# Optimization experiments

Hardware: AMD Instinct MI355X
Metric: run time of the kernel (lower is better)

## Reference

```python
import jax, jax.numpy as jnp
import numpy as np

B, C, L, M, EMB, HID = 32, 64, 8192, 32, 256, 64

def setup_inputs() -> dict:
    key = jax.random.key(0)
    ks = jax.random.split(key, 14)
    s_w = 1.0 / (C * C)
    s_a = 1.0 / EMB
    return {
        "x": jax.random.normal(ks[0], (B, C, L), jnp.float32),
        "emb": jax.random.normal(ks[1], (B, EMB), jnp.float32),
        "weights_pos": s_w * jax.random.normal(ks[2], (C, C, M, 2), jnp.float32),
        "weights_neg": s_w * jax.random.normal(ks[3], (C, C, M, 2), jnp.float32),
        "A_real_pos": s_a * jax.random.normal(ks[4], (M, EMB), jnp.float32),
        "A_imag_pos": s_a * jax.random.normal(ks[5], (M, EMB), jnp.float32),
        "A_real_neg": s_a * jax.random.normal(ks[6], (M, EMB), jnp.float32),
        "A_imag_neg": s_a * jax.random.normal(ks[7], (M, EMB), jnp.float32),
        "tm_w1": 0.05 * jax.random.normal(ks[8], (HID, EMB), jnp.float32),
        "tm_b1": jnp.zeros((HID,), jnp.float32),
        "tm_w2": 0.05 * jax.random.normal(ks[9], (2 * C, HID), jnp.float32),
        "tm_b2": jnp.zeros((2 * C,), jnp.float32),
        "lin_w": 0.05 * jax.random.normal(ks[10], (C, C), jnp.float32),
        "lin_b": jnp.zeros((C,), jnp.float32),
    }

def reference(x, emb, weights_pos, weights_neg, A_real_pos, A_imag_pos,
              A_real_neg, A_imag_neg, tm_w1, tm_b1, tm_w2, tm_b2, lin_w, lin_b):
    b, c, l = x.shape
    m = weights_pos.shape[2]
    k = l // 2 + 1
    # ---- SpectralConv1d branch ----
    x_ft = jnp.fft.rfft(x, norm="ortho")  # [B,C,K] complex
    wp = weights_pos[..., 0] + 1j * weights_pos[..., 1]  # [Ci,Co,M]
    wn = weights_neg[..., 0] + 1j * weights_neg[..., 1]
    phi_p = (emb @ A_real_pos.T) + 1j * (emb @ A_imag_pos.T)  # [B,M]
    phi_n = (emb @ A_real_neg.T) + 1j * (emb @ A_imag_neg.T)
    out_pos = jnp.einsum("bim,iom->bom", x_ft[:, :, :m], wp) * phi_p[:, None, :]
    out_neg = jnp.einsum("bim,iom->bom", x_ft[:, :, k - m:], wn) * phi_n[:, None, :]
    out_ft = jnp.zeros((b, c, k), dtype=x_ft.dtype)
    out_ft = out_ft.at[:, :, :m].set(out_pos).at[:, :, k - m:].set(out_neg)
    x1 = jnp.fft.irfft(out_ft, n=l, norm="ortho")  # [B,C,L]
    # ---- Conv1DTime branch (FiLM-style) ----
    h = jax.nn.silu(emb @ tm_w1.T + tm_b1)          # [B,HID]
    gb = h @ tm_w2.T + tm_b2                         # [B,2C]
    gamma, beta = gb[:, :c], gb[:, c:]
    xl = jnp.einsum("bcl,oc->bol", x, lin_w) + lin_b[None, :, None]
    x2 = xl * (1.0 + gamma[:, :, None]) + beta[:, :, None]
    return jax.nn.silu(x1 + x2)
```

## Files before the change

### kernel.cpp

```cpp
#include <hip/hip_runtime.h>
#include <math.h>

#define L_ 8192
#define EMB_ 256
#define HID_ 64

typedef __attribute__((ext_vector_type(8))) short bf16x8;
typedef __attribute__((ext_vector_type(4))) float f32x4;
typedef __attribute__((ext_vector_type(4))) int i32x4;

#define OFF_TFB  0
#define OFF_TLB  262144
#define OFF_AFB  524288
#define OFF_XFRP 917504
#define OFF_B2   3014656
#define OFF_PHI  3016704
#define OFF_GB   3020800
#define OFF_WT   3024896
#define OFF_XT   3549184

__device__ inline int pkbf(float a, float b) {
    int r;
    asm volatile("v_cvt_pk_bf16_f32 %0, %1, %2" : "=v"(r) : "v"(a), "v"(b));
    return r;
}
__device__ inline bf16x8 asbf(i32x4 v) { union { i32x4 i; bf16x8 h; } u; u.i = v; return u.h; }
#define MFMA(A,B,C) __builtin_amdgcn_mfma_f32_16x16x32_bf16((A),(B),(C),0,0,0)

__device__ inline ushort f2bf(float v) {
    unsigned b = __float_as_uint(v);
    return (ushort)((b + 0x7FFFu + ((b >> 16) & 1u)) >> 16);
}
__device__ inline float bf2f(ushort h) { return __uint_as_float(((unsigned)h) << 16); }
__device__ inline float hwsin(float rev) { float r; asm("v_sin_f32 %0, %1" : "=v"(r) : "v"(rev)); return r; }
__device__ inline float hwcos(float rev) { float r; asm("v_cos_f32 %0, %1" : "=v"(r) : "v"(rev)); return r; }
__device__ inline unsigned permb(unsigned hi, unsigned lo, unsigned sel) {
    unsigned r;
    asm("v_perm_b32 %0, %1, %2, %3" : "=v"(r) : "v"(hi), "v"(lo), "v"(sel));
    return r;
}

__global__ __launch_bounds__(256) void k_init(ushort* __restrict__ TLB, ushort* __restrict__ TFB,
        const float* __restrict__ emb,
        const float* __restrict__ Arp, const float* __restrict__ Aip,
        const float* __restrict__ Arn, const float* __restrict__ Ain, float* __restrict__ phi,
        const float* __restrict__ w1, const float* __restrict__ b1,
        const float* __restrict__ w2, const float* __restrict__ b2, float* __restrict__ gb,
        const float* __restrict__ wpos, const float* __restrict__ wneg, float* __restrict__ WT) {
    int bid = blockIdx.x;
    if (bid < 4096) {
        int idx = bid * 256 + threadIdx.x;
        int f, l; ushort* dst;
        if (idx < 524288) {
            int u = idx;
            int e = u & 7, lane = (u >> 3) & 63, ct = (u >> 9) & 3, kstep = u >> 11;
            l = kstep * 32 + ((lane >> 4) << 3) + e;
            f = ct * 16 + (lane & 15);
            dst = TLB + u;
        } else {
            int u = idx - 524288;
            int e = u & 7, lane = (u >> 3) & 63, ts = (u >> 9) & 1, lt = u >> 10;
            l = lt * 16 + (lane & 15);
            f = ts * 32 + ((lane >> 4) << 3) + e;
            dst = TFB + u;
        }
        int fr = f & 31; bool sinp = (f & 32) != 0;
        int r = (fr * l) & (L_ - 1);
        float rev = (float)r * (1.0f / (float)L_);
        float v = sinp ? hwsin(rev) : hwcos(rev);
        *dst = f2bf(v);
    } else if (bid < 4112) {
        int tid = (bid - 4096) * 256 + threadIdx.x;
        int b = tid >> 7;
        int mm = (tid >> 2) & 31;
        int cmp = tid & 3;
        const float* A = (cmp == 0) ? Arp : (cmp == 1) ? Aip : (cmp == 2) ? Arn : Ain;
        const float4* e4 = (const float4*)(emb + b * EMB_);
        const float4* a4 = (const float4*)(A + mm * EMB_);
        float acc = 0.f;
        for (int q = 0; q < EMB_ / 4; ++q) {
            float4 ev = e4[q], av = a4[q];
            acc += ev.x * av.x + ev.y * av.y + ev.z * av.z + ev.w * av.w;
        }
        phi[tid] = acc;
    } else if (bid < 4144) {
        __shared__ float h[HID_];
        int b = bid - 4112, t = threadIdx.x;
        if (t < HID_) {
            const float4* e4 = (const float4*)(emb + b * EMB_);
            const float4* w4 = (const float4*)(w1 + t * EMB_);
            float acc = b1[t];
            for (int q = 0; q < EMB_ / 4; ++q) {
                float4 ev = e4[q], wv = w4[q];
                acc += ev.x * wv.x + ev.y * wv.y + ev.z * wv.z + ev.w * wv.w;
            }
            h[t] = acc / (1.f + expf(-acc));
        }
        __syncthreads();
        if (t < 128) {
            float g = b2[t];
            const float4* h4 = (const float4*)h;
            const float4* w4 = (const float4*)(w2 + t * HID_);
            for (int q = 0; q < HID_ / 4; ++q) {
                float4 hv = h4[q], wv = w4[q];
                g += hv.x * wv.x + hv.y * wv.y + hv.z * wv.z + hv.w * wv.w;
            }
            if (t < 64) gb[(b * 64 + t) * 2 + 0] = 1.f + g;
            else        gb[(b * 64 + (t - 64)) * 2 + 1] = g;
        }
    } else {
        int t = bid - 4144;
        int side = t >> 6, i = t & 63;
        const float* W = side ? wneg : wpos;
        const float* src = W + (size_t)i * 4096;
        int tid = threadIdx.x;
        #pragma unroll
        for (int j = 0; j < 8; ++j) {
            int u = tid + 256 * j;
            int mm = u >> 6, o = u & 63;
            float2 v = *(const float2*)(src + o * 64 + mm * 2);
            *(float2*)(WT + ((size_t)(side * 32 + mm)) * 8192 + i * 128 + o * 2) = v;
        }
    }
}

__global__ __launch_bounds__(256, 4) void k_dft(const float* __restrict__ x,
        const ushort* __restrict__ TLB, float* __restrict__ xfrp, unsigned* __restrict__ XT2) {
    __shared__ float sP[4][16][132];
    int stripe = blockIdx.x >> 3;
    int lseg = blockIdx.x & 7;
    int w = threadIdx.x >> 6;
    int lane = threadIdx.x & 63;
    int row = lane & 15, koff = (lane >> 4) << 3;
    int r0 = stripe * 16;
    int kb0 = lseg * 1024 + w * 256;

    f32x4 acc[8];
    #pragma unroll
    for (int i = 0; i < 8; ++i) acc[i] = (f32x4){0.f, 0.f, 0.f, 0.f};

    const float* ap = x + (size_t)(r0 + row) * L_ + kb0 + koff;
    const i32x4* tb = (const i32x4*)TLB;
    int tbase = (kb0 >> 5) * 256 + lane;
    const i32x4 SM = {(int)0x80000000, (int)0x80000000, (int)0x80000000, (int)0x80000000};
    unsigned* xtb = XT2 + ((size_t)stripe * 4096 + ((kb0 + koff) >> 1)) * 16 + row;

    float4 xa0 = *(const float4*)(ap);
    float4 xc0 = *(const float4*)(ap + 4);
    float4 xa1 = *(const float4*)(ap + 32);
    float4 xc1 = *(const float4*)(ap + 36);
    float4 xa2 = *(const float4*)(ap + 64);
    float4 xc2 = *(const float4*)(ap + 68);
    i32x4 t0 = tb[tbase], t1 = tb[tbase + 64], t2 = tb[tbase + 128], t3 = tb[tbase + 192];
    i32x4 u0 = tb[tbase + 256], u1 = tb[tbase + 320], u2 = tb[tbase + 384], u3 = tb[tbase + 448];
    #pragma unroll
    for (int ks = 0; ks < 8; ++ks) {
        float4 nxa = {0,0,0,0}, nxc = {0,0,0,0};
        i32x4 v0 = u0, v1 = u1, v2 = u2, v3 = u3;
        if (ks < 5) {
            nxa = *(const float4*)(ap + (ks + 3) * 32);
            nxc = *(const float4*)(ap + (ks + 3) * 32 + 4);
        }
        if (ks < 6) {
            int ti = tbase + (ks + 2) * 256;
            v0 = tb[ti]; v1 = tb[ti + 64]; v2 = tb[ti + 128]; v3 = tb[ti + 192];
        }
        int h0 = pkbf(xa0.x, xa0.y), h1 = pkbf(xa0.z, xa0.w);
        int h2 = pkbf(xc0.x, xc0.y), h3 = pkbf(xc0.z, xc0.w);
        bf16x8 AH = asbf((i32x4){h0, h1, h2, h3});
        acc[0] = MFMA(AH, asbf(t0), acc[0]); acc[4] = MFMA(AH, asbf(t0 ^ SM), acc[4]);
        acc[1] = MFMA(AH, asbf(t1), acc[1]); acc[5] = MFMA(AH, asbf(t1 ^ SM), acc[5]);
        acc[2] = MFMA(AH, asbf(t2), acc[2]); acc[6] = MFMA(AH, asbf(t2 ^ SM), acc[6]);
        acc[3] = MFMA(AH, asbf(t3), acc[3]); acc[7] = MFMA(AH, asbf(t3 ^ SM), acc[7]);
        {
            unsigned* xtp = xtb + (size_t)(ks * 16) * 16;
            xtp[0]  = (unsigned)h0;
            xtp[16] = (unsigned)h1;
            xtp[32] = (unsigned)h2;
            xtp[48] = (unsigned)h3;
        }
        xa0 = xa1; xc0 = xc1; xa1 = xa2; xc1 = xc2; xa2 = nxa; xc2 = nxc;
        t0 = u0; t1 = u1; t2 = u2; t3 = u3;
        u0 = v0; u1 = v1; u2 = v2; u3 = v3;
    }
    int crow = (lane >> 4) << 2;
    int ccol = lane & 15;
    #pragma unroll
    for (int ct = 0; ct < 8; ++ct)
        #pragma unroll
        for (int r = 0; r < 4; ++r)
            sP[w][crow + r][ct * 16 + ccol] = acc[ct][r];
    __syncthreads();
    #pragma unroll
    for (int i = 0; i < 8; ++i) {
        int e = threadIdx.x + 256 * i;
        int rr = e & 15, cc = e >> 4;
        float s = sP[0][rr][cc] + sP[1][rr][cc] + sP[2][rr][cc] + sP[3][rr][cc];
        xfrp[((size_t)(lseg * 128 + cc)) * 2048 + r0 + rr] = s;
    }
}

__global__ __launch_bounds__(256) void k_mix(const float* __restrict__ xfrt,
        const float* __restrict__ WT,
        const float* __restrict__ phi, const float* __restrict__ lw,
        const float* __restrict__ lb, const float* __restrict__ gb,
        ushort* __restrict__ afb, float* __restrict__ bias2) {
    int bi = blockIdx.x;
    int tid = threadIdx.x;
    if (bi >= 256) {
        int b = bi - 256;
        ushort* dst = afb + (size_t)b * 24576;
        #pragma unroll
        for (int j = 0; j < 16; ++j) {
            int u = tid + 256 * j;
            int e = u & 7, lane = (u >> 3) & 63, mt = (u >> 9) & 3, ks2 = u >> 11;
            int c = mt * 16 + (lane & 15);
            int kk = ((lane >> 4) << 3) + e;
            float v = lw[c * 64 + ks2 * 32 + kk] * gb[(b * 64 + c) * 2];
            ushort hi = f2bf(v);
            int base = (((4 + ks2) * 4 + mt) * 64 + lane) * 16;
            dst[base + e] = hi;
            dst[base + 8 + e] = f2bf(v - bf2f(hi));
        }
        if (tid < 64) {
            float g1 = gb[(b * 64 + tid) * 2], be = gb[(b * 64 + tid) * 2 + 1];
            bias2[b * 64 + tid] = lb[tid] * g1 + be;
        }
        return;
    }
    __shared__ float sW[64][64][2];
    __shared__ float sXr[8][64], sXi[8][64];
    int bh = bi & 3, side = (bi >> 2) & 1, mm = bi >> 3;
    int slot = side ? (31 - mm) : mm;
    int colR = side ? (64 + slot) : mm;
    int colI = side ? (96 + slot) : (32 + mm);

    {
        const float4* wt = (const float4*)(WT + ((size_t)(side * 32 + mm)) * 8192);
        float* sWlin = &sW[0][0][0];
        #pragma unroll
        for (int j = 0; j < 8; ++j) {
            int u = tid + 256 * j;
            *(float4*)&sWlin[u * 4] = wt[u];
        }
    }
    {
        const float2* pR = (const float2*)(xfrt + (size_t)colR * 2048 + bh * 512);
        const float2* pI = (const float2*)(xfrt + (size_t)colI * 2048 + bh * 512);
        float2 aR = {0, 0}, aI = {0, 0};
        #pragma unroll
        for (int s = 0; s < 8; ++s) {
            float2 vR = pR[(size_t)s * 131072 + tid];
            float2 vI = pI[(size_t)s * 131072 + tid];
            aR.x += vR.x; aR.y += vR.y;
            aI.x += vI.x; aI.y += vI.y;
        }
        if (!side) { aI.x = -aI.x; aI.y = -aI.y; }
        *(float2*)&sXr[tid >> 5][(tid & 31) * 2] = aR;
        *(float2*)&sXi[tid >> 5][(tid & 31) * 2] = aI;
    }
    __syncthreads();

    int o = tid & 63, bg = tid >> 6;
    const float invL = 1.f / (float)L_;
    float fac = (slot == 0) ? invL : 2.f * invL;
    int comp = side ? 2 : 0;
    int e = slot & 7, kgrp = slot >> 3;
    int mt = o >> 4, lane = kgrp * 16 + (o & 15);
    #pragma unroll
    for (int bl = 0; bl < 2; ++bl) {
        int b_local = bg * 2 + bl;
        int b = bh * 8 + b_local;
        float sre = 0.f, sim = 0.f;
        #pragma unroll 16
        for (int i = 0; i < 64; ++i) {
            float wr = sW[i][o][0], wi = sW[i][o][1];
            float xr = sXr[b_local][i], xi = sXi[b_local][i];
            sre += xr * wr - xi * wi;
            sim += xr * wi + xi * wr;
        }
        const float* ph = &phi[(b * 32 + mm) * 4 + (side ? 2 : 0)];
        float phr = ph[0], phim = ph[1];
        float Pre = sre * phr - sim * phim;
        float Pim = sre * phim + sim * phr;
        float a = fac * Pre;
        float bcoef = (slot == 0) ? 0.f : (side ? 2.f * invL * Pim : -2.f * invL * Pim);
        ushort* dst = afb + (size_t)b * 24576;
        ushort hiA = f2bf(a);
        int baseA = ((comp * 4 + mt) * 64 + lane) * 16;
        dst[baseA + e] = hiA;
        dst[baseA + 8 + e] = f2bf(a - bf2f(hiA));
        ushort hiB = f2bf(bcoef);
        int baseB = (((comp + 1) * 4 + mt) * 64 + lane) * 16;
        dst[baseB + e] = hiB;
        dst[baseB + 8 + e] = f2bf(bcoef - bf2f(hiB));
    }
}

#define TPART(ts)                                                                        \
    {                                                                                    \
        i32x4 bh_[2];                                                                    \
        _Pragma("unroll")                                                                \
        for (int nj = 0; nj < 2; ++nj)                                                   \
            bh_[nj] = tb[((lt0 + nj) * 2 + (ts)) * 64 + lane];                           \
        _Pragma("unroll")                                                                \
        for (int mt = 0; mt < 4; ++mt) {                                                 \
            i32x4 ah0 = ab[(((ts) * 4 + mt) * 64 + lane) * 2];                           \
            i32x4 ah1 = ab[(((2 + (ts)) * 4 + mt) * 64 + lane) * 2];                     \
            bf16x8 AH0 = asbf(ah0), AH1 = asbf(ah1);                                     \
            _Pragma("unroll")                                                            \
            for (int nj = 0; nj < 2; ++nj) {                                             \
                acc[mt][nj] = MFMA(AH0, asbf(bh_[nj]), acc[mt][nj]);                     \
                acc[mt][nj] = MFMA(AH1, asbf(bh_[nj] ^ SM), acc[mt][nj]);                \
            }                                                                            \
        }                                                                                \
    }

#define XPART(ts, xv0, xv1)                                                              \
    {                                                                                    \
        bf16x8 XH0 = asbf(xv0), XH1 = asbf(xv1);                                         \
        _Pragma("unroll")                                                                \
        for (int mt = 0; mt < 4; ++mt) {                                                 \
            i32x4 ah = ab[(((4 + (ts)) * 4 + mt) * 64 + lane) * 2];                      \
            bf16x8 AH = asbf(ah);                                                        \
            acc[mt][0] = MFMA(AH, XH0, acc[mt][0]);                                      \
            acc[mt][1] = MFMA(AH, XH1, acc[mt][1]);                                      \
        }                                                                                \
    }

#define XEXTRACT(q0, q1, dstvar)                                                         \
    dstvar = (i32x4){                                                                    \
        (int)permb((unsigned)q0[1], (unsigned)q0[0], sel),                               \
        (int)permb((unsigned)q0[3], (unsigned)q0[2], sel),                               \
        (int)permb((unsigned)q1[1], (unsigned)q1[0], sel),                               \
        (int)permb((unsigned)q1[3], (unsigned)q1[2], sel)};

__global__ __launch_bounds__(256, 3) void k_fuse(const unsigned* __restrict__ XT2,
        const ushort* __restrict__ TFB, const ushort* __restrict__ AFB,
        const float* __restrict__ bias2, float* __restrict__ out) {
    int b = blockIdx.x >> 6, lt = blockIdx.x & 63;
    int w = threadIdx.x >> 6, lane = threadIdx.x & 63;
    int col = lane & 15, kgrp = lane >> 4;
    int lbase = lt * 128 + w * 32;
    int lt0 = lbase >> 4;
    const i32x4* tb = (const i32x4*)TFB;
    const i32x4* ab = (const i32x4*)AFB + (size_t)b * 3072;
    const i32x4* xt4 = (const i32x4*)XT2;

    f32x4 acc[4][2];
    #pragma unroll
    for (int i = 0; i < 4; ++i)
        #pragma unroll
        for (int j = 0; j < 2; ++j) acc[i][j] = (f32x4){0.f, 0.f, 0.f, 0.f};

    int sm = (col & 1) ? (int)0x80008000 : 0;
    i32x4 SM = {sm, sm, sm, sm};
    unsigned sel = (col & 1) ? 0x07060302u : 0x05040100u;

    size_t i00 = ((size_t)(b * 4 + (kgrp >> 1)) * 4096 + ((lbase + col) >> 1)) * 4 + (kgrp & 1) * 2;
    size_t i01 = i00 + 8 * 4;
    size_t i10 = i00 + (size_t)2 * 4096 * 4;
    size_t i11 = i10 + 8 * 4;
    i32x4 q000 = xt4[i00], q001 = xt4[i00 + 1];
    i32x4 q010 = xt4[i01], q011 = xt4[i01 + 1];
    i32x4 q100 = xt4[i10], q101 = xt4[i10 + 1];
    i32x4 q110 = xt4[i11], q111 = xt4[i11 + 1];

    TPART(0)
    i32x4 xv00, xv01;
    XEXTRACT(q000, q001, xv00)
    XEXTRACT(q010, q011, xv01)
    XPART(0, xv00, xv01)
    TPART(1)
    i32x4 xv10, xv11;
    XEXTRACT(q100, q101, xv10)
    XEXTRACT(q110, q111, xv11)
    XPART(1, xv10, xv11)

    #pragma unroll
    for (int mt = 0; mt < 4; ++mt) {
        #pragma unroll
        for (int r = 0; r < 4; ++r) {
            int c = mt * 16 + kgrp * 4 + r;
            float bias = bias2[b * 64 + c];
            float* op = out + (size_t)(b * 64 + c) * L_ + lbase + col;
            #pragma unroll
            for (int nj = 0; nj < 2; ++nj) {
                float v = acc[mt][nj][r] + bias;
                op[nj * 16] = v / (1.f + __expf(-v));
            }
        }
    }
}

extern "C" void kernel_launch(void* const* d_in, const int* in_sizes, int n_in,
                              void* d_out, int out_size, void* d_ws, size_t ws_size,
                              hipStream_t stream) {
    const float* x    = (const float*)d_in[0];
    const float* emb  = (const float*)d_in[1];
    const float* wpos = (const float*)d_in[2];
    const float* wneg = (const float*)d_in[3];
    const float* Arp  = (const float*)d_in[4];
    const float* Aip  = (const float*)d_in[5];
    const float* Arn  = (const float*)d_in[6];
    const float* Ain  = (const float*)d_in[7];
    const float* w1   = (const float*)d_in[8];
    const float* b1   = (const float*)d_in[9];
    const float* w2   = (const float*)d_in[10];
    const float* b2   = (const float*)d_in[11];
    const float* lw   = (const float*)d_in[12];
    const float* lb   = (const float*)d_in[13];
    float* out = (float*)d_out;
    float* ws = (float*)d_ws;
    ushort*   TFB  = (ushort*)(ws + OFF_TFB);
    ushort*   TLB  = (ushort*)(ws + OFF_TLB);
    ushort*   AFB  = (ushort*)(ws + OFF_AFB);
    float*    XFRP = ws + OFF_XFRP;
    float*    B2   = ws + OFF_B2;
    float*    PHI  = ws + OFF_PHI;
    float*    GB   = ws + OFF_GB;
    float*    WT   = ws + OFF_WT;
    unsigned* XT2  = (unsigned*)(ws + OFF_XT);

    hipLaunchKernelGGL(k_init,  dim3(4272), dim3(256), 0, stream,
                       TLB, TFB, emb, Arp, Aip, Arn, Ain, PHI, w1, b1, w2, b2, GB,
                       wpos, wneg, WT);
    hipLaunchKernelGGL(k_dft,   dim3(1024), dim3(256), 0, stream, x, TLB, XFRP, XT2);
    hipLaunchKernelGGL(k_mix,   dim3(288),  dim3(256), 0, stream, XFRP, WT, PHI,
                       lw, lb, GB, AFB, B2);
    hipLaunchKernelGGL(k_fuse,  dim3(2048), dim3(256), 0, stream, XT2, TFB, AFB, B2, out);
}
```

Measured before the change: 66.43 us.

## Retile DFT kernel to two row stripes per block sharing twiddle loads

Each k_dft block now handles 32 rows (two 16-row stripes) over a 512-wide L segment instead of 16 rows over 1024. Each twiddle-table fragment loaded from memory now feeds MFMAs for both stripes, halving twiddle traffic per row. The price is twice as many L segments (16 instead of 8), so the partial-sum buffer doubles, workspace offsets shift, and k_mix must sum 16 partials instead of 8. The kernel also doubles accumulator registers and drops the deeper software prefetch of twiddles.

Measured after the change: 74.83 us. 1.13x slower.

```diff
diff --git a/kernel.cpp b/kernel.cpp
--- a/kernel.cpp
+++ b/kernel.cpp
@@ -13,11 +13,11 @@
 #define OFF_TLB  262144
 #define OFF_AFB  524288
 #define OFF_XFRP 917504
-#define OFF_B2   3014656
-#define OFF_PHI  3016704
-#define OFF_GB   3020800
-#define OFF_WT   3024896
-#define OFF_XT   3549184
+#define OFF_B2   5111808
+#define OFF_PHI  5113856
+#define OFF_GB   5117952
+#define OFF_WT   5122048
+#define OFF_XT   5646336
 
 __device__ inline int pkbf(float a, float b) {
     int r;
@@ -127,61 +127,67 @@
 __global__ __launch_bounds__(256, 4) void k_dft(const float* __restrict__ x,
         const ushort* __restrict__ TLB, float* __restrict__ xfrp, unsigned* __restrict__ XT2) {
     __shared__ float sP[4][16][132];
-    int stripe = blockIdx.x >> 3;
-    int lseg = blockIdx.x & 7;
+    int rowgrp = blockIdx.x >> 4;
+    int lseg = blockIdx.x & 15;
     int w = threadIdx.x >> 6;
     int lane = threadIdx.x & 63;
     int row = lane & 15, koff = (lane >> 4) << 3;
-    int r0 = stripe * 16;
-    int kb0 = lseg * 1024 + w * 256;
-
-    f32x4 acc[8];
-    #pragma unroll
-    for (int i = 0; i < 8; ++i) acc[i] = (f32x4){0.f, 0.f, 0.f, 0.f};
-
-    const float* ap = x + (size_t)(r0 + row) * L_ + kb0 + koff;
+    int r0 = rowgrp * 32;
+    int kb0 = lseg * 512 + w * 128;
+
+    f32x4 acc0[8], acc1[8];
+    #pragma unroll
+    for (int i = 0; i < 8; ++i) {
+        acc0[i] = (f32x4){0.f, 0.f, 0.f, 0.f};
+        acc1[i] = (f32x4){0.f, 0.f, 0.f, 0.f};
+    }
+
+    const float* ap0 = x + (size_t)(r0 + row) * L_ + kb0 + koff;
+    const float* ap1 = ap0 + (size_t)16 * L_;
     const i32x4* tb = (const i32x4*)TLB;
     int tbase = (kb0 >> 5) * 256 + lane;
     const i32x4 SM = {(int)0x80000000, (int)0x80000000, (int)0x80000000, (int)0x80000000};
-    unsigned* xtb = XT2 + ((size_t)stripe * 4096 + ((kb0 + koff) >> 1)) * 16 + row;
-
-    float4 xa0 = *(const float4*)(ap);
-    float4 xc0 = *(const float4*)(ap + 4);
-    float4 xa1 = *(const float4*)(ap + 32);
-    float4 xc1 = *(const float4*)(ap + 36);
-    float4 xa2 = *(const float4*)(ap + 64);
-    float4 xc2 = *(const float4*)(ap + 68);
-    i32x4 t0 = tb[tbase], t1 = tb[tbase + 64], t2 = tb[tbase + 128], t3 = tb[tbase + 192];
-    i32x4 u0 = tb[tbase + 256], u1 = tb[tbase + 320], u2 = tb[tbase + 384], u3 = tb[tbase + 448];
-    #pragma unroll
-    for (int ks = 0; ks < 8; ++ks) {
-        float4 nxa = {0,0,0,0}, nxc = {0,0,0,0};
-        i32x4 v0 = u0, v1 = u1, v2 = u2, v3 = u3;
-        if (ks < 5) {
-            nxa = *(const float4*)(ap + (ks + 3) * 32);
-            nxc = *(const float4*)(ap + (ks + 3) * 32 + 4);
-        }
-        if (ks < 6) {
-            int ti = tbase + (ks + 2) * 256;
-            v0 = tb[ti]; v1 = tb[ti + 64]; v2 = tb[ti + 128]; v3 = tb[ti + 192];
-        }
-        int h0 = pkbf(xa0.x, xa0.y), h1 = pkbf(xa0.z, xa0.w);
-        int h2 = pkbf(xc0.x, xc0.y), h3 = pkbf(xc0.z, xc0.w);
-        bf16x8 AH = asbf((i32x4){h0, h1, h2, h3});
-        acc[0] = MFMA(AH, asbf(t0), acc[0]); acc[4] = MFMA(AH, asbf(t0 ^ SM), acc[4]);
-        acc[1] = MFMA(AH, asbf(t1), acc[1]); acc[5] = MFMA(AH, asbf(t1 ^ SM), acc[5]);
-        acc[2] = MFMA(AH, asbf(t2), acc[2]); acc[6] = MFMA(AH, asbf(t2 ^ SM), acc[6]);
-        acc[3] = MFMA(AH, asbf(t3), acc[3]); acc[7] = MFMA(AH, asbf(t3 ^ SM), acc[7]);
+    unsigned* xtb0 = XT2 + ((size_t)(rowgrp * 2) * 4096 + ((kb0 + koff) >> 1)) * 16 + row;
+    unsigned* xtb1 = xtb0 + (size_t)4096 * 16;
+
+    float4 a0c = *(const float4*)(ap0);
+    float4 c0c = *(const float4*)(ap0 + 4);
+    float4 a1c = *(const float4*)(ap1);
+    float4 c1c = *(const float4*)(ap1 + 4);
+    #pragma unroll
+    for (int ks = 0; ks < 4; ++ks) {
+        float4 a0n = {0,0,0,0}, c0n = {0,0,0,0}, a1n = {0,0,0,0}, c1n = {0,0,0,0};
+        if (ks < 3) {
+            a0n = *(const float4*)(ap0 + (ks + 1) * 32);
+            c0n = *(const float4*)(ap0 + (ks + 1) * 32 + 4);
+            a1n = *(const float4*)(ap1 + (ks + 1) * 32);
+            c1n = *(const float4*)(ap1 + (ks + 1) * 32 + 4);
+        }
+        int ti = tbase + ks * 256;
+        i32x4 t0 = tb[ti], t1 = tb[ti + 64], t2 = tb[ti + 128], t3 = tb[ti + 192];
+        int h00 = pkbf(a0c.x, a0c.y), h01 = pkbf(a0c.z, a0c.w);
+        int h02 = pkbf(c0c.x, c0c.y), h03 = pkbf(c0c.z, c0c.w);
+        int h10 = pkbf(a1c.x, a1c.y), h11 = pkbf(a1c.z, a1c.w);
+        int h12 = pkbf(c1c.x, c1c.y), h13 = pkbf(c1c.z, c1c.w);
+        bf16x8 A0 = asbf((i32x4){h00, h01, h02, h03});
+        bf16x8 A1 = asbf((i32x4){h10, h11, h12, h13});
         {
-            unsigned* xtp = xtb + (size_t)(ks * 16) * 16;
-            xtp[0]  = (unsigned)h0;
-            xtp[16] = (unsigned)h1;
-            xtp[32] = (unsigned)h2;
-            xtp[48] = (unsigned)h3;
-        }
-        xa0 = xa1; xc0 = xc1; xa1 = xa2; xc1 = xc2; xa2 = nxa; xc2 = nxc;
-        t0 = u0; t1 = u1; t2 = u2; t3 = u3;
-        u0 = v0; u1 = v1; u2 = v2; u3 = v3;
+            unsigned* p0 = xtb0 + (size_t)(ks * 16) * 16;
+            p0[0]  = (unsigned)h00; p0[16] = (unsigned)h01;
+            p0[32] = (unsigned)h02; p0[48] = (unsigned)h03;
+            unsigned* p1 = xtb1 + (size_t)(ks * 16) * 16;
+            p1[0]  = (unsigned)h10; p1[16] = (unsigned)h11;
+            p1[32] = (unsigned)h12; p1[48] = (unsigned)h13;
+        }
+        acc0[0] = MFMA(A0, asbf(t0), acc0[0]); acc0[4] = MFMA(A0, asbf(t0 ^ SM), acc0[4]);
+        acc0[1] = MFMA(A0, asbf(t1), acc0[1]); acc0[5] = MFMA(A0, asbf(t1 ^ SM), acc0[5]);
+        acc0[2] = MFMA(A0, asbf(t2), acc0[2]); acc0[6] = MFMA(A0, asbf(t2 ^ SM), acc0[6]);
+        acc0[3] = MFMA(A0, asbf(t3), acc0[3]); acc0[7] = MFMA(A0, asbf(t3 ^ SM), acc0[7]);
+        acc1[0] = MFMA(A1, asbf(t0), acc1[0]); acc1[4] = MFMA(A1, asbf(t0 ^ SM), acc1[4]);
+        acc1[1] = MFMA(A1, asbf(t1), acc1[1]); acc1[5] = MFMA(A1, asbf(t1 ^ SM), acc1[5]);
+        acc1[2] = MFMA(A1, asbf(t2), acc1[2]); acc1[6] = MFMA(A1, asbf(t2 ^ SM), acc1[6]);
+        acc1[3] = MFMA(A1, asbf(t3), acc1[3]); acc1[7] = MFMA(A1, asbf(t3 ^ SM), acc1[7]);
+        a0c = a0n; c0c = c0n; a1c = a1n; c1c = c1n;
     }
     int crow = (lane >> 4) << 2;
     int ccol = lane & 15;
@@ -189,7 +195,7 @@
     for (int ct = 0; ct < 8; ++ct)
         #pragma unroll
         for (int r = 0; r < 4; ++r)
-            sP[w][crow + r][ct * 16 + ccol] = acc[ct][r];
+            sP[w][crow + r][ct * 16 + ccol] = acc0[ct][r];
     __syncthreads();
     #pragma unroll
     for (int i = 0; i < 8; ++i) {
@@ -197,6 +203,20 @@
         int rr = e & 15, cc = e >> 4;
         float s = sP[0][rr][cc] + sP[1][rr][cc] + sP[2][rr][cc] + sP[3][rr][cc];
         xfrp[((size_t)(lseg * 128 + cc)) * 2048 + r0 + rr] = s;
+    }
+    __syncthreads();
+    #pragma unroll
+    for (int ct = 0; ct < 8; ++ct)
+        #pragma unroll
+        for (int r = 0; r < 4; ++r)
+            sP[w][crow + r][ct * 16 + ccol] = acc1[ct][r];
+    __syncthreads();
+    #pragma unroll
+    for (int i = 0; i < 8; ++i) {
+        int e = threadIdx.x + 256 * i;
+        int rr = e & 15, cc = e >> 4;
+        float s = sP[0][rr][cc] + sP[1][rr][cc] + sP[2][rr][cc] + sP[3][rr][cc];
+        xfrp[((size_t)(lseg * 128 + cc)) * 2048 + r0 + 16 + rr] = s;
     }
 }
 
@@ -249,7 +269,7 @@
         const float2* pI = (const float2*)(xfrt + (size_t)colI * 2048 + bh * 512);
         float2 aR = {0, 0}, aI = {0, 0};
         #pragma unroll
-        for (int s = 0; s < 8; ++s) {
+        for (int s = 0; s < 16; ++s) {
             float2 vR = pR[(size_t)s * 131072 + tid];
             float2 vI = pI[(size_t)s * 131072 + tid];
             aR.x += vR.x; aR.y += vR.y;
```
